# Kernel optimization log

Hardware: AMD Instinct MI355X
Metric: run time of the kernel (lower is better)

The kernel has to match this reference:

```python
import jax, jax.numpy as jnp
import numpy as np

B, S, D = 4, 2048, 768
H = 12
HD = D // H  # 64


def setup_inputs() -> dict:
    key = jax.random.key(0)
    k1, k2, k3 = jax.random.split(key, 3)
    return {
        "hidden_states": jax.random.normal(k1, (B, S, D), dtype=jnp.float32),
        "W_attn": jax.random.normal(k2, (D, 3 * D), dtype=jnp.float32) * 0.02,
        "b_attn": jnp.zeros((3 * D,), dtype=jnp.float32),
        "W_proj": jax.random.normal(k3, (D, D), dtype=jnp.float32) * 0.02,
        "b_proj": jnp.zeros((D,), dtype=jnp.float32),
    }


def reference(hidden_states, W_attn, b_attn, W_proj, b_proj):
    # Conv1D c_attn: x @ W + b -> [B, S, 3D]
    qkv = hidden_states @ W_attn + b_attn
    q, k, v = jnp.split(qkv, 3, axis=-1)

    def split_heads(t):
        # [B, S, D] -> [B, H, S, HD]
        return t.reshape(B, S, H, HD).transpose(0, 2, 1, 3)

    q, k, v = split_heads(q), split_heads(k), split_heads(v)

    # attn_weights = q @ k^T / sqrt(head_dim); NOTE: this module variant applies
    # no causal mask when attention_mask is None (faithful to source _attn).
    scale = jnp.asarray(HD, dtype=q.dtype) ** 0.5
    scores = jnp.einsum("bhqd,bhkd->bhqk", q, k) / scale
    weights = jax.nn.softmax(scores, axis=-1)

    attn = jnp.einsum("bhqk,bhkd->bhqd", weights, v)
    # merge heads -> [B, S, D]
    attn = attn.transpose(0, 2, 1, 3).reshape(B, S, D)
    # Conv1D c_proj
    out = attn @ W_proj + b_proj
    return out
```

## Files before the change

### kernel.cpp

```cpp
#include <hip/hip_runtime.h>

typedef short short8 __attribute__((ext_vector_type(8)));
typedef float f32x2 __attribute__((ext_vector_type(2)));
typedef float f32x4 __attribute__((ext_vector_type(4)));
typedef float f32x16 __attribute__((ext_vector_type(16)));

__device__ __forceinline__ unsigned short f2bf(float f){
  union { float f; unsigned int u; } x; x.f = f;
  unsigned int r = x.u + 0x7fffu + ((x.u >> 16) & 1u);
  return (unsigned short)(r >> 16);
}

__device__ __forceinline__ void gload_lds16(const void* g, void* l){
  __builtin_amdgcn_global_load_lds(
      (const __attribute__((address_space(1))) void*)g,
      (__attribute__((address_space(3))) void*)l, 16, 0, 0);
}

__device__ __forceinline__ unsigned int cvtpk_bf16(float lo, float hi){
  unsigned int r;
  asm("v_cvt_pk_bf16_f32 %0, %1, %2" : "=v"(r) : "v"(lo), "v"(hi));
  return r;
}

__device__ __forceinline__ f32x2 pk_add(f32x2 a, f32x2 b){
  f32x2 d;
  asm("v_pk_add_f32 %0, %1, %2" : "=v"(d) : "v"(a), "v"(b));
  return d;
}

__global__ __launch_bounds__(256) void cast_f32_bf16(const float* __restrict__ in,
                                                     unsigned short* __restrict__ out, int n4){
  int i = blockIdx.x * blockDim.x + threadIdx.x;
  const int stride = gridDim.x * blockDim.x;
  for (; i < n4; i += stride){
    float4 v = ((const float4*)in)[i];
    ushort4 o;
    o.x = f2bf(v.x); o.y = f2bf(v.y); o.z = f2bf(v.z); o.w = f2bf(v.w);
    ((ushort4*)out)[i] = o;
  }
}

__global__ __launch_bounds__(256) void transpose_to_bf16(const float* __restrict__ W,
                                                         unsigned short* __restrict__ WT,
                                                         int K, int N){
  __shared__ float tile[64][68];
  const int n0 = blockIdx.x * 64, k0 = blockIdx.y * 64;
  const int t = threadIdx.x;
  const int qn = (t & 15) * 4;
  #pragma unroll
  for (int i = 0; i < 4; ++i){
    const int kk = (t >> 4) + i * 16;
    float4 v = *(const float4*)&W[(size_t)(k0 + kk) * N + n0 + qn];
    tile[kk][qn + 0] = v.x; tile[kk][qn + 1] = v.y;
    tile[kk][qn + 2] = v.z; tile[kk][qn + 3] = v.w;
  }
  __syncthreads();
  const int qk = (t & 15) * 4;
  #pragma unroll
  for (int i = 0; i < 4; ++i){
    const int nn = (t >> 4) + i * 16;
    ushort4 o;
    o.x = f2bf(tile[qk + 0][nn]); o.y = f2bf(tile[qk + 1][nn]);
    o.z = f2bf(tile[qk + 2][nn]); o.w = f2bf(tile[qk + 3][nn]);
    *(ushort4*)&WT[(size_t)(n0 + nn) * K + k0 + qk] = o;
  }
}

__global__ __launch_bounds__(256) void gemm_qkv(const unsigned short* __restrict__ A,
                                                const unsigned short* __restrict__ Bt,
                                                const float* __restrict__ bias,
                                                unsigned short* __restrict__ qkv){
  __shared__ unsigned short As[2][128 * 32];
  __shared__ unsigned short Bs[2][128 * 32];
  const int tid = threadIdx.x;
  const int wave = tid >> 6, lane = tid & 63;
  const int g = lane >> 4, l15 = lane & 15;
  const int wr = wave >> 1, wc = wave & 1;
  const int d = blockIdx.x;
  const int w = (d & 7) * 144 + (d >> 3);
  const int m0 = (w / 18) * 128, n0 = (w % 18) * 128;

  f32x4 acc[4][4] = {};

  auto stage = [&](int bi, int kt){
    const int k0 = kt * 32;
    #pragma unroll
    for (int c = 0; c < 2; ++c){
      const int z = c * 4096 + tid * 16;
      const int r = z >> 6;
      const int ys = (z & 63) ^ ((r & 3) << 4);
      gload_lds16((const char*)A + ((size_t)(m0 + r) * 768 + k0) * 2 + ys,
                  (char*)&As[bi][0] + c * 4096 + wave * 1024);
      gload_lds16((const char*)Bt + ((size_t)(n0 + r) * 768 + k0) * 2 + ys,
                  (char*)&Bs[bi][0] + c * 4096 + wave * 1024);
    }
  };

  stage(0, 0);
  for (int kt = 0; kt < 24; ++kt){
    __syncthreads();
    if (kt + 1 < 24) stage((kt + 1) & 1, kt + 1);
    const char* Ab = (const char*)&As[kt & 1][0];
    const char* Bb = (const char*)&Bs[kt & 1][0];
    short8 a[4], b[4];
    #pragma unroll
    for (int mt = 0; mt < 4; ++mt){
      const int row = wr * 64 + mt * 16 + l15;
      a[mt] = *(const short8*)(Ab + row * 64 + ((g * 16) ^ ((row & 3) << 4)));
    }
    #pragma unroll
    for (int nt = 0; nt < 4; ++nt){
      const int row = wc * 64 + nt * 16 + l15;
      b[nt] = *(const short8*)(Bb + row * 64 + ((g * 16) ^ ((row & 3) << 4)));
    }
    #pragma unroll
    for (int mt = 0; mt < 4; ++mt)
      #pragma unroll
      for (int nt = 0; nt < 4; ++nt)
        acc[mt][nt] = __builtin_amdgcn_mfma_f32_16x16x32_bf16(a[mt], b[nt], acc[mt][nt], 0, 0, 0);
  }

  #pragma unroll
  for (int nt = 0; nt < 4; ++nt){
    const int n = n0 + wc * 64 + nt * 16 + l15;
    const int which = n / 768;
    const float bs = bias[n];
    if (which == 2){
      const int hd = n & 63;
      const int head = (n - 1536) >> 6;
      #pragma unroll
      for (int mt = 0; mt < 4; ++mt){
        const int m = m0 + wr * 64 + mt * 16 + 4 * g;
        const int bb = m >> 11, sidx = m & 2047;
        unsigned short* dst = qkv + (size_t)2 * 6291456 +
                              ((size_t)(bb * 12 + head) * 64 + hd) * 2048 + sidx;
        #pragma unroll
        for (int rp = 0; rp < 2; ++rp){
          const unsigned int lo = f2bf(acc[mt][nt][2 * rp] + bs);
          const unsigned int hi = f2bf(acc[mt][nt][2 * rp + 1] + bs);
          *(unsigned int*)(dst + 2 * rp) = lo | (hi << 16);
        }
      }
    } else {
      const int h2 = (n - which * 768) >> 6;
      const int hd = n & 63;
      const float sc = (which == 0) ? 0.18033688f : 1.0f;
      #pragma unroll
      for (int mt = 0; mt < 4; ++mt)
        #pragma unroll
        for (int r = 0; r < 4; ++r){
          const int m = m0 + wr * 64 + mt * 16 + 4 * g + r;
          const int bb = m >> 11, sidx = m & 2047;
          qkv[(size_t)which * 6291456u +
              ((((size_t)bb * 12 + h2) * 2048 + sidx) * 64 + hd)] = f2bf((acc[mt][nt][r] + bs) * sc);
        }
    }
  }
}

__global__ __launch_bounds__(256) void gemm_proj(const unsigned short* __restrict__ A,
                                                 const unsigned short* __restrict__ Bt,
                                                 const float* __restrict__ bias,
                                                 float* __restrict__ out){
  __shared__ unsigned short As[2][128 * 32];
  __shared__ unsigned short Bs[2][64 * 32];
  const int tid = threadIdx.x;
  const int wave = tid >> 6, lane = tid & 63;
  const int g = lane >> 4, l15 = lane & 15;
  const int d = blockIdx.x;
  const int w = (d & 7) * 96 + (d >> 3);
  const int m0 = (w / 12) * 128, n0 = (w % 12) * 64;

  f32x4 acc[2][4] = {};

  auto stage = [&](int bi, int kt){
    const int k0 = kt * 32;
    #pragma unroll
    for (int c = 0; c < 2; ++c){
      const int z = c * 4096 + tid * 16;
      const int r = z >> 6;
      const int ys = (z & 63) ^ ((r & 3) << 4);
      gload_lds16((const char*)A + ((size_t)(m0 + r) * 768 + k0) * 2 + ys,
                  (char*)&As[bi][0] + c * 4096 + wave * 1024);
    }
    const int z = tid * 16;
    const int r = z >> 6;
    const int ys = (z & 63) ^ ((r & 3) << 4);
    gload_lds16((const char*)Bt + ((size_t)(n0 + r) * 768 + k0) * 2 + ys,
                (char*)&Bs[bi][0] + wave * 1024);
  };

  stage(0, 0);
  for (int kt = 0; kt < 24; ++kt){
    __syncthreads();
    if (kt + 1 < 24) stage((kt + 1) & 1, kt + 1);
    const char* Ab = (const char*)&As[kt & 1][0];
    const char* Bb = (const char*)&Bs[kt & 1][0];
    short8 a[2], b[4];
    #pragma unroll
    for (int mt = 0; mt < 2; ++mt){
      const int row = wave * 32 + mt * 16 + l15;
      a[mt] = *(const short8*)(Ab + row * 64 + ((g * 16) ^ ((row & 3) << 4)));
    }
    #pragma unroll
    for (int nt = 0; nt < 4; ++nt){
      const int row = nt * 16 + l15;
      b[nt] = *(const short8*)(Bb + row * 64 + ((g * 16) ^ ((row & 3) << 4)));
    }
    #pragma unroll
    for (int mt = 0; mt < 2; ++mt)
      #pragma unroll
      for (int nt = 0; nt < 4; ++nt)
        acc[mt][nt] = __builtin_amdgcn_mfma_f32_16x16x32_bf16(a[mt], b[nt], acc[mt][nt], 0, 0, 0);
  }

  #pragma unroll
  for (int mt = 0; mt < 2; ++mt)
    #pragma unroll
    for (int nt = 0; nt < 4; ++nt){
      const int n = n0 + nt * 16 + l15;
      const float bs = bias[n];
      #pragma unroll
      for (int r = 0; r < 4; ++r){
        const int m = m0 + wave * 32 + mt * 16 + 4 * g + r;
        out[(size_t)m * 768 + n] = acc[mt][nt][r] + bs;
      }
    }
}

__global__ __launch_bounds__(256) void attn_fwd5(const unsigned short* __restrict__ qw,
                                                 const unsigned short* __restrict__ kw,
                                                 const unsigned short* __restrict__ vtw,
                                                 unsigned short* __restrict__ aout){
  __shared__ unsigned short Ks[2][64 * 64];
  __shared__ unsigned short Vs[2][64 * 64];
  __shared__ float bcast[4][32];
  const int tid = threadIdx.x;
  const int wave = tid >> 6, lane = tid & 63;
  const int h = lane >> 5, ql = lane & 31;
  const int dd = blockIdx.x;
  const int wk = (dd & 7) * 96 + (dd >> 3);
  const int bh = wk >> 4;
  const int q0 = (wk & 15) * 128 + wave * 32;
  const size_t base = (size_t)bh * 2048 * 64;

  short8 qf[4];
  #pragma unroll
  for (int c = 0; c < 4; ++c)
    qf[c] = *(const short8*)(qw + base + (size_t)(q0 + ql) * 64 + c * 16 + h * 8);

  f32x16 acc[2] = {};
  float lsum = 0.f;

  auto stageKV = [&](int bi, int t){
    #pragma unroll
    for (int c = 0; c < 2; ++c){
      const int z = c * 4096 + tid * 16;
      const int r = z >> 7, y = z & 127;
      const int ys = y ^ ((r & 7) << 4);
      gload_lds16((const char*)kw + (base + (size_t)(t * 64 + r) * 64) * 2 + ys,
                  (char*)&Ks[bi][0] + z);
      gload_lds16((const char*)vtw + (base + (size_t)r * 2048 + t * 64) * 2 + ys,
                  (char*)&Vs[bi][0] + z);
    }
  };

  stageKV(0, 0);
  __syncthreads();

  for (int t = 0; t < 32; ++t){
    const int buf = t & 1;
    if (t + 1 < 32) stageKV(buf ^ 1, t + 1);

    f32x16 s[2] = {};
    #pragma unroll
    for (int kt = 0; kt < 2; ++kt)
      #pragma unroll
      for (int c = 0; c < 4; ++c){
        const int row = kt * 32 + ql;
        short8 af = *(const short8*)((const char*)&Ks[buf][0] + row * 128 +
                                     ((c * 32 + h * 16) ^ ((row & 7) << 4)));
        s[kt] = __builtin_amdgcn_mfma_f32_32x32x16_bf16(af, qf[c], s[kt], 0, 0, 0);
      }

    #pragma unroll
    for (int kt = 0; kt < 2; ++kt)
      #pragma unroll
      for (int r = 0; r < 16; ++r)
        s[kt][r] = __builtin_amdgcn_exp2f(s[kt][r]);

    {
      f32x2 a0 = pk_add(__builtin_shufflevector(s[0], s[0], 0, 1),  __builtin_shufflevector(s[0], s[0], 2, 3));
      f32x2 a1 = pk_add(__builtin_shufflevector(s[0], s[0], 4, 5),  __builtin_shufflevector(s[0], s[0], 6, 7));
      f32x2 a2 = pk_add(__builtin_shufflevector(s[0], s[0], 8, 9),  __builtin_shufflevector(s[0], s[0], 10, 11));
      f32x2 a3 = pk_add(__builtin_shufflevector(s[0], s[0], 12, 13), __builtin_shufflevector(s[0], s[0], 14, 15));
      f32x2 b0 = pk_add(__builtin_shufflevector(s[1], s[1], 0, 1),  __builtin_shufflevector(s[1], s[1], 2, 3));
      f32x2 b1 = pk_add(__builtin_shufflevector(s[1], s[1], 4, 5),  __builtin_shufflevector(s[1], s[1], 6, 7));
      f32x2 b2 = pk_add(__builtin_shufflevector(s[1], s[1], 8, 9),  __builtin_shufflevector(s[1], s[1], 10, 11));
      f32x2 b3 = pk_add(__builtin_shufflevector(s[1], s[1], 12, 13), __builtin_shufflevector(s[1], s[1], 14, 15));
      a0 = pk_add(a0, a1); a2 = pk_add(a2, a3);
      b0 = pk_add(b0, b1); b2 = pk_add(b2, b3);
      a0 = pk_add(a0, a2); b0 = pk_add(b0, b2);
      a0 = pk_add(a0, b0);
      lsum += a0[0] + a0[1];
    }

    #pragma unroll
    for (int kt = 0; kt < 2; ++kt){
      unsigned int w0 = cvtpk_bf16(s[kt][0],  s[kt][1]),  x0 = cvtpk_bf16(s[kt][4],  s[kt][5]);
      asm("v_permlane32_swap_b32 %0, %1" : "+v"(w0), "+v"(x0));
      unsigned int w1 = cvtpk_bf16(s[kt][2],  s[kt][3]),  x1 = cvtpk_bf16(s[kt][6],  s[kt][7]);
      asm("v_permlane32_swap_b32 %0, %1" : "+v"(w1), "+v"(x1));
      unsigned int w2 = cvtpk_bf16(s[kt][8],  s[kt][9]),  x2 = cvtpk_bf16(s[kt][12], s[kt][13]);
      asm("v_permlane32_swap_b32 %0, %1" : "+v"(w2), "+v"(x2));
      unsigned int w3 = cvtpk_bf16(s[kt][10], s[kt][11]), x3 = cvtpk_bf16(s[kt][14], s[kt][15]);
      asm("v_permlane32_swap_b32 %0, %1" : "+v"(w3), "+v"(x3));
      union { unsigned int u[4]; short8 v; } pa2[2];
      pa2[0].u[0] = w0; pa2[0].u[1] = w1; pa2[0].u[2] = x0; pa2[0].u[3] = x1;
      pa2[1].u[0] = w2; pa2[1].u[1] = w3; pa2[1].u[2] = x2; pa2[1].u[3] = x3;
      #pragma unroll
      for (int c2 = 0; c2 < 2; ++c2){
        const int kc = kt * 2 + c2;
        #pragma unroll
        for (int ht = 0; ht < 2; ++ht){
          const int row = ht * 32 + ql;
          short8 vb = *(const short8*)((const char*)&Vs[buf][0] + row * 128 +
                                       ((kc * 32 + h * 16) ^ ((row & 7) << 4)));
          acc[ht] = __builtin_amdgcn_mfma_f32_32x32x16_bf16(pa2[c2].v, vb, acc[ht], 0, 0, 0);
        }
      }
    }

    __syncthreads();
  }

  lsum += __shfl_xor(lsum, 32);
  if (h == 0) bcast[wave][ql] = 1.0f / lsum;
  const int bb = bh / 12, hh = bh % 12;
  #pragma unroll
  for (int g4 = 0; g4 < 4; ++g4){
    float4 f4 = *(const float4*)&bcast[wave][8 * g4 + 4 * h];
    #pragma unroll
    for (int j = 0; j < 4; ++j){
      const int row = 8 * g4 + 4 * h + j;
      const float li = ((const float*)&f4)[j];
      #pragma unroll
      for (int ht = 0; ht < 2; ++ht)
        aout[(size_t)(bb * 2048 + q0 + row) * 768 + hh * 64 + ht * 32 + ql] =
            f2bf(acc[ht][4 * g4 + j] * li);
    }
  }
}

extern "C" void kernel_launch(void* const* d_in, const int* in_sizes, int n_in,
                              void* d_out, int out_size, void* d_ws, size_t ws_size,
                              hipStream_t stream){
  const float* hs = (const float*)d_in[0];
  const float* Wa = (const float*)d_in[1];
  const float* ba = (const float*)d_in[2];
  const float* Wp = (const float*)d_in[3];
  const float* bp = (const float*)d_in[4];

  char* ws = (char*)d_ws;
  unsigned short* hbf = (unsigned short*)ws;
  unsigned short* WaT = (unsigned short*)(ws + 12582912);
  unsigned short* WpT = (unsigned short*)(ws + 12582912 + 3538944);
  unsigned short* qkv = (unsigned short*)(ws + 12582912 + 3538944 + 1179648);
  unsigned short* abf = qkv + (size_t)3 * 6291456;

  cast_f32_bf16<<<dim3(2048), dim3(256), 0, stream>>>(hs, hbf, 8192 * 768 / 4);
  transpose_to_bf16<<<dim3(36, 12), dim3(256), 0, stream>>>(Wa, WaT, 768, 2304);
  transpose_to_bf16<<<dim3(12, 12), dim3(256), 0, stream>>>(Wp, WpT, 768, 768);
  gemm_qkv<<<dim3(1152), dim3(256), 0, stream>>>(hbf, WaT, ba, qkv);
  attn_fwd5<<<dim3(768), dim3(256), 0, stream>>>(qkv, qkv + 6291456, qkv + (size_t)2 * 6291456, abf);
  gemm_proj<<<dim3(768), dim3(256), 0, stream>>>(abf, WpT, bp, (float*)d_out);
}
```

Before: 154.7 us.

## Fuse prep kernels into one launch and halve attention block size

The cast kernel and the two weight-transpose kernels are merged into one launch that picks its job from the block index, which removes two kernel launches. The attention kernel now runs 2 waves (128 threads) per block over 64 query rows, with twice as many blocks, and each thread stages four KV chunks instead of two. This raises the number of resident blocks and spreads the work more finely, but each K/V tile staged in LDS is now reused by fewer query rows. The per-row 1/lsum broadcast now uses lane shuffles instead of shared memory.

```diff
diff --git a/kernel.cpp b/kernel.cpp
--- a/kernel.cpp
+++ b/kernel.cpp
@@ -29,24 +29,36 @@
   return d;
 }
 
-__global__ __launch_bounds__(256) void cast_f32_bf16(const float* __restrict__ in,
-                                                     unsigned short* __restrict__ out, int n4){
-  int i = blockIdx.x * blockDim.x + threadIdx.x;
-  const int stride = gridDim.x * blockDim.x;
-  for (; i < n4; i += stride){
-    float4 v = ((const float4*)in)[i];
-    ushort4 o;
-    o.x = f2bf(v.x); o.y = f2bf(v.y); o.z = f2bf(v.z); o.w = f2bf(v.w);
-    ((ushort4*)out)[i] = o;
-  }
-}
-
-__global__ __launch_bounds__(256) void transpose_to_bf16(const float* __restrict__ W,
-                                                         unsigned short* __restrict__ WT,
-                                                         int K, int N){
+__global__ __launch_bounds__(256) void prep_fused(const float* __restrict__ hs,
+                                                  unsigned short* __restrict__ hbf,
+                                                  const float* __restrict__ Wa,
+                                                  unsigned short* __restrict__ WaT,
+                                                  const float* __restrict__ Wp,
+                                                  unsigned short* __restrict__ WpT){
   __shared__ float tile[64][68];
-  const int n0 = blockIdx.x * 64, k0 = blockIdx.y * 64;
+  const int b = blockIdx.x;
   const int t = threadIdx.x;
+  if (b < 2048){
+    const int n4 = 8192 * 768 / 4;
+    int i = b * 256 + t;
+    for (; i < n4; i += 2048 * 256){
+      float4 v = ((const float4*)hs)[i];
+      ushort4 o;
+      o.x = f2bf(v.x); o.y = f2bf(v.y); o.z = f2bf(v.z); o.w = f2bf(v.w);
+      ((ushort4*)hbf)[i] = o;
+    }
+    return;
+  }
+  const float* W; unsigned short* WT; int K, N, n0, k0;
+  if (b < 2480){
+    const int idx = b - 2048;
+    W = Wa; WT = WaT; K = 768; N = 2304;
+    n0 = (idx % 36) * 64; k0 = (idx / 36) * 64;
+  } else {
+    const int idx = b - 2480;
+    W = Wp; WT = WpT; K = 768; N = 768;
+    n0 = (idx % 12) * 64; k0 = (idx / 12) * 64;
+  }
   const int qn = (t & 15) * 4;
   #pragma unroll
   for (int i = 0; i < 4; ++i){
@@ -229,20 +241,19 @@
     }
 }
 
-__global__ __launch_bounds__(256) void attn_fwd5(const unsigned short* __restrict__ qw,
+__global__ __launch_bounds__(128) void attn_fwd6(const unsigned short* __restrict__ qw,
                                                  const unsigned short* __restrict__ kw,
                                                  const unsigned short* __restrict__ vtw,
                                                  unsigned short* __restrict__ aout){
   __shared__ unsigned short Ks[2][64 * 64];
   __shared__ unsigned short Vs[2][64 * 64];
-  __shared__ float bcast[4][32];
   const int tid = threadIdx.x;
   const int wave = tid >> 6, lane = tid & 63;
   const int h = lane >> 5, ql = lane & 31;
   const int dd = blockIdx.x;
-  const int wk = (dd & 7) * 96 + (dd >> 3);
-  const int bh = wk >> 4;
-  const int q0 = (wk & 15) * 128 + wave * 32;
+  const int wk = (dd & 7) * 192 + (dd >> 3);
+  const int bh = wk >> 5;
+  const int q0 = (wk & 31) * 64 + wave * 32;
   const size_t base = (size_t)bh * 2048 * 64;
 
   short8 qf[4];
@@ -255,8 +266,8 @@
 
   auto stageKV = [&](int bi, int t){
     #pragma unroll
-    for (int c = 0; c < 2; ++c){
-      const int z = c * 4096 + tid * 16;
+    for (int c = 0; c < 4; ++c){
+      const int z = c * 2048 + tid * 16;
       const int r = z >> 7, y = z & 127;
       const int ys = y ^ ((r & 7) << 4);
       gload_lds16((const char*)kw + (base + (size_t)(t * 64 + r) * 64) * 2 + ys,
@@ -336,21 +347,19 @@
   }
 
   lsum += __shfl_xor(lsum, 32);
-  if (h == 0) bcast[wave][ql] = 1.0f / lsum;
+  const float inv = 1.0f / lsum;
   const int bb = bh / 12, hh = bh % 12;
   #pragma unroll
-  for (int g4 = 0; g4 < 4; ++g4){
-    float4 f4 = *(const float4*)&bcast[wave][8 * g4 + 4 * h];
+  for (int g4 = 0; g4 < 4; ++g4)
     #pragma unroll
     for (int j = 0; j < 4; ++j){
       const int row = 8 * g4 + 4 * h + j;
-      const float li = ((const float*)&f4)[j];
+      const float li = __shfl(inv, row);
       #pragma unroll
       for (int ht = 0; ht < 2; ++ht)
         aout[(size_t)(bb * 2048 + q0 + row) * 768 + hh * 64 + ht * 32 + ql] =
             f2bf(acc[ht][4 * g4 + j] * li);
     }
-  }
 }
 
 extern "C" void kernel_launch(void* const* d_in, const int* in_sizes, int n_in,
@@ -369,10 +378,8 @@
   unsigned short* qkv = (unsigned short*)(ws + 12582912 + 3538944 + 1179648);
   unsigned short* abf = qkv + (size_t)3 * 6291456;
 
-  cast_f32_bf16<<<dim3(2048), dim3(256), 0, stream>>>(hs, hbf, 8192 * 768 / 4);
-  transpose_to_bf16<<<dim3(36, 12), dim3(256), 0, stream>>>(Wa, WaT, 768, 2304);
-  transpose_to_bf16<<<dim3(12, 12), dim3(256), 0, stream>>>(Wp, WpT, 768, 768);
+  prep_fused<<<dim3(2624), dim3(256), 0, stream>>>(hs, hbf, Wa, WaT, Wp, WpT);
   gemm_qkv<<<dim3(1152), dim3(256), 0, stream>>>(hbf, WaT, ba, qkv);
-  attn_fwd5<<<dim3(768), dim3(256), 0, stream>>>(qkv, qkv + 6291456, qkv + (size_t)2 * 6291456, abf);
+  attn_fwd6<<<dim3(1536), dim3(128), 0, stream>>>(qkv, qkv + 6291456, qkv + (size_t)2 * 6291456, abf);
   gemm_proj<<<dim3(768), dim3(256), 0, stream>>>(abf, WpT, bp, (float*)d_out);
 }
```

Result: slower. 173.2 us (+11.9%).
